# Performance work log

Hardware: AMD Instinct MI355X
Metric: run time of the kernel (lower is better)

Reference implementation:

```python
import jax, jax.numpy as jnp
import numpy as np

N_NODES = 20000
N_EDGES = 320000
X_DIM = 128
EDGE_DIM = 64
HIDDEN = 256
OUT_DIM = 256
LAYERS = 3
N_GRAPHS = 64


def setup_inputs() -> dict:
    key = jax.random.key(0)
    ks = jax.random.split(key, 20)
    x = jax.random.normal(ks[0], (N_NODES, X_DIM), dtype=jnp.float32)
    edge_index = jax.random.randint(ks[1], (2, N_EDGES), 0, N_NODES, dtype=jnp.int64)
    edge_attr = jax.random.normal(ks[2], (N_EDGES, EDGE_DIM), dtype=jnp.float32)
    batch_ids = jnp.sort(jax.random.randint(ks[3], (N_NODES,), 0, N_GRAPHS, dtype=jnp.int64))

    def lin(k, fan_in, fan_out):
        bound = 1.0 / np.sqrt(fan_in)
        kw, kb = jax.random.split(k)
        W = jax.random.uniform(kw, (fan_in, fan_out), minval=-bound, maxval=bound, dtype=jnp.float32)
        b = jax.random.uniform(kb, (fan_out,), minval=-bound, maxval=bound, dtype=jnp.float32)
        return W, b

    xproj_W, xproj_b = lin(ks[4], X_DIM, HIDDEN)
    edge_W, edge_b, mlp_W1, mlp_b1, mlp_W2, mlp_b2 = [], [], [], [], [], []
    for l in range(LAYERS):
        eW, eb = lin(ks[5 + l], EDGE_DIM, HIDDEN)
        w1, b1 = lin(ks[8 + l], HIDDEN, HIDDEN)
        w2, b2 = lin(ks[11 + l], HIDDEN, HIDDEN)
        edge_W.append(eW); edge_b.append(eb)
        mlp_W1.append(w1); mlp_b1.append(b1)
        mlp_W2.append(w2); mlp_b2.append(b2)
    out_W1, out_b1 = lin(ks[14], HIDDEN, HIDDEN)
    out_W2, out_b2 = lin(ks[15], HIDDEN, OUT_DIM)
    return {
        "x": x, "edge_index": edge_index, "edge_attr": edge_attr, "batch_ids": batch_ids,
        "xproj_W": xproj_W, "xproj_b": xproj_b,
        "edge_W": jnp.stack(edge_W), "edge_b": jnp.stack(edge_b),
        "mlp_W1": jnp.stack(mlp_W1), "mlp_b1": jnp.stack(mlp_b1),
        "mlp_W2": jnp.stack(mlp_W2), "mlp_b2": jnp.stack(mlp_b2),
        "out_W1": out_W1, "out_b1": out_b1, "out_W2": out_W2, "out_b2": out_b2,
    }


def reference(x, edge_index, edge_attr, batch_ids, xproj_W, xproj_b,
              edge_W, edge_b, mlp_W1, mlp_b1, mlp_W2, mlp_b2,
              out_W1, out_b1, out_W2, out_b2):
    src, dst = edge_index[0], edge_index[1]
    h = x @ xproj_W + xproj_b  # [N, H]
    for l in range(LAYERS):
        # GINE message: relu(x_j + Lin(edge_attr)), aggregated by sum at target
        msg = jax.nn.relu(h[src] + edge_attr @ edge_W[l] + edge_b[l])  # [E, H]
        agg = jax.ops.segment_sum(msg, dst, num_segments=N_NODES)      # [N, H]
        z = h + agg  # (1 + eps) * x_i with eps = 0
        z = jax.nn.relu(z @ mlp_W1[l] + mlp_b1[l]) @ mlp_W2[l] + mlp_b2[l]
        h = jax.nn.relu(z)  # outer F.relu in forward
    # global mean pool over graphs
    sums = jax.ops.segment_sum(h, batch_ids, num_segments=N_GRAPHS)    # [G, H]
    counts = jax.ops.segment_sum(jnp.ones((h.shape[0],), h.dtype), batch_ids, num_segments=N_GRAPHS)
    g = sums / jnp.maximum(counts, 1.0)[:, None]
    g = jax.nn.relu(g @ out_W1 + out_b1) @ out_W2 + out_b2
    # F.normalize(dim=-1): x / max(||x||_2, eps)
    norm = jnp.maximum(jnp.linalg.norm(g, axis=-1, keepdims=True), 1e-12)
    return g / norm
```

## Files before the change

kernel.cpp:

```cpp
#include <hip/hip_runtime.h>

#define N_NODES 20000
#define N_EDGES 320000
#define X_DIM 128
#define EDGE_DIM 64
#define HIDDEN 256
#define N_GRAPHS 64
#define LAYERS 3

#define NPB 8
#define EB 32
#define ET 4
#define PSPLIT 8
#define NBLK ((N_NODES + 255) / 256)

typedef __attribute__((ext_vector_type(8))) short short8;
typedef __attribute__((ext_vector_type(4))) float floatx4;

__device__ __forceinline__ unsigned short f2bf(float f) {
    union { float f; unsigned u; } v; v.f = f;
    return (unsigned short)((v.u + 0x7FFFu + ((v.u >> 16) & 1u)) >> 16);
}
__device__ __forceinline__ float bf2f(unsigned short u) {
    return __uint_as_float(((unsigned)u) << 16);
}


__global__ __launch_bounds__(256) void deg_kernel(const int* __restrict__ ei,
                                                  int* __restrict__ deg)
{
    int e = blockIdx.x * 256 + threadIdx.x;
    if (e < N_EDGES) atomicAdd(&deg[ei[N_EDGES + e]], 1);
}

__global__ __launch_bounds__(256) void pscan_kernel(const int* __restrict__ deg,
                                                    int* __restrict__ rp,
                                                    int* __restrict__ bsum)
{
    __shared__ int buf[256];
    const int t = threadIdx.x;
    const int i = blockIdx.x * 256 + t;
    int v = (i < N_NODES) ? deg[i] : 0;
    buf[t] = v;
    __syncthreads();
    for (int off = 1; off < 256; off <<= 1) {
        int a = (t >= off) ? buf[t - off] : 0;
        __syncthreads();
        buf[t] += a;
        __syncthreads();
    }
    if (i < N_NODES) rp[i] = buf[t] - v;
    if (t == 255) bsum[blockIdx.x] = buf[255];
}

__global__ __launch_bounds__(128) void bscan_kernel(const int* __restrict__ bsum,
                                                    int* __restrict__ boff)
{
    __shared__ int buf[128];
    const int t = threadIdx.x;
    int v = (t < NBLK) ? bsum[t] : 0;
    buf[t] = v;
    __syncthreads();
    for (int off = 1; off < 128; off <<= 1) {
        int a = (t >= off) ? buf[t - off] : 0;
        __syncthreads();
        buf[t] += a;
        __syncthreads();
    }
    if (t < NBLK) boff[t] = buf[t] - v;
}

__global__ __launch_bounds__(256) void addoff_kernel(int* __restrict__ rp,
                                                     const int* __restrict__ boff)
{
    const int i = blockIdx.x * 256 + threadIdx.x;
    if (i < N_NODES) rp[i] += boff[blockIdx.x];
    if (i == 0) rp[N_NODES] = N_EDGES;
}

__global__ __launch_bounds__(256) void scatter_kernel(const int* __restrict__ ei,
                                                      const int* __restrict__ rp,
                                                      int* __restrict__ cursor,
                                                      int* __restrict__ perm)
{
    const int e = blockIdx.x * 256 + threadIdx.x;
    if (e < N_EDGES) {
        const int d = ei[N_EDGES + e];
        const int pos = atomicAdd(&cursor[d], 1);
        perm[rp[d] + pos] = e;
    }
}

__global__ __launch_bounds__(256) void permute_kernel(
    const float* __restrict__ ea, const int* __restrict__ ei,
    const int* __restrict__ perm, unsigned short* __restrict__ eab,
    int* __restrict__ srcs, int* __restrict__ dsts)
{
    const int tid = blockIdx.x * 256 + threadIdx.x;
    const int e = tid >> 3, seg = tid & 7;
    const int p = perm[e];
    const float* sp = ea + (size_t)p * EDGE_DIM + seg * 8;
    const float4 v0 = *(const float4*)sp;
    const float4 v1 = *(const float4*)(sp + 4);
    short8 o;
    o[0] = (short)f2bf(v0.x); o[1] = (short)f2bf(v0.y);
    o[2] = (short)f2bf(v0.z); o[3] = (short)f2bf(v0.w);
    o[4] = (short)f2bf(v1.x); o[5] = (short)f2bf(v1.y);
    o[6] = (short)f2bf(v1.z); o[7] = (short)f2bf(v1.w);
    *(short8*)(eab + (size_t)e * EDGE_DIM + seg * 8) = o;
    if (seg == 0) { srcs[e] = ei[p]; dsts[e] = ei[N_EDGES + p]; }
}

__global__ __launch_bounds__(256) void swizzle_kernel(const float* __restrict__ W,
                                                      unsigned short* __restrict__ out,
                                                      int KK)
{
    const int i = blockIdx.x * 256 + threadIdx.x;
    if (i >= 8192 * KK) return;
    const int j = i & 7, lane = (i >> 3) & 63, rem = i >> 9;
    const int kk = rem % KK, rem2 = rem / KK, nt = rem2 & 3, wvv = rem2 >> 2;
    const int n = wvv * 64 + nt * 16 + (lane & 15);
    const int k = kk * 32 + (lane >> 4) * 8 + j;
    out[i] = f2bf(W[k * HIDDEN + n]);
}


__global__ __launch_bounds__(256) void node_proj_kernel(
    const float* __restrict__ x, const float* __restrict__ W,
    const float* __restrict__ b, float* __restrict__ h,
    unsigned short* __restrict__ hbf, float* __restrict__ z)
{
    const int t = threadIdx.x;
    const int row0 = blockIdx.x * NPB;
    __shared__ float xs[NPB][X_DIM];
    for (int idx = t; idx < NPB * X_DIM; idx += 256)
        xs[idx / X_DIM][idx % X_DIM] = x[(size_t)row0 * X_DIM + idx];
    __syncthreads();
    float acc[NPB];
    const float bt = b[t];
#pragma unroll
    for (int r = 0; r < NPB; r++) acc[r] = bt;
    for (int k = 0; k < X_DIM; k++) {
        const float wv = W[k * HIDDEN + t];
#pragma unroll
        for (int r = 0; r < NPB; r++) acc[r] += xs[r][k] * wv;
    }
#pragma unroll
    for (int r = 0; r < NPB; r++) {
        const size_t idx = (size_t)(row0 + r) * HIDDEN + t;
        h[idx] = acc[r];
        hbf[idx] = f2bf(acc[r]);
        z[idx] = 0.f;
    }
}

__global__ __launch_bounds__(256, 4) void edge_mfma_kernel(
    const unsigned short* __restrict__ eab, const int* __restrict__ srcs,
    const int* __restrict__ dsts, const unsigned short* __restrict__ Ws,
    const float* __restrict__ b, const unsigned short* __restrict__ hbf,
    float* __restrict__ z)
{
    const int t = threadIdx.x;
    const int lane = t & 63, wv = t >> 6, q = lane >> 4, m15 = lane & 15;
    __shared__ unsigned short msg[EB][264];
    __shared__ int s_src[2][EB], s_dst[2][EB];

    short8 bfr[4][2];
#pragma unroll
    for (int nt = 0; nt < 4; nt++)
#pragma unroll
        for (int kk = 0; kk < 2; kk++)
            bfr[nt][kk] = *(const short8*)(Ws + ((((wv * 4 + nt) * 2 + kk) * 64) + lane) * 8);
    const float bt = b[t];

    if (t < EB) {
        const int e0 = blockIdx.x * ET * EB;
        s_src[0][t] = srcs[e0 + t];
        s_dst[0][t] = dsts[e0 + t];
    }
    __syncthreads();

    float s = 0.f;
    int prev = s_dst[0][0];

    for (int tile = 0; tile < ET; tile++) {
        const int cur = tile & 1;
        const int e0 = (blockIdx.x * ET + tile) * EB;

        unsigned short hv[EB];
#pragma unroll
        for (int e = 0; e < EB; e++)
            hv[e] = hbf[(size_t)s_src[cur][e] * HIDDEN + t];

        if (tile + 1 < ET && t < EB) {
            s_src[1 - cur][t] = srcs[e0 + EB + t];
            s_dst[1 - cur][t] = dsts[e0 + EB + t];
        }

        floatx4 acc[2][4];
#pragma unroll
        for (int mt = 0; mt < 2; mt++)
#pragma unroll
            for (int nt = 0; nt < 4; nt++)
                acc[mt][nt] = (floatx4){0.f, 0.f, 0.f, 0.f};
#pragma unroll
        for (int kk = 0; kk < 2; kk++) {
            const short8 a0 = *(const short8*)(eab + (size_t)(e0 + m15) * EDGE_DIM + kk * 32 + q * 8);
            const short8 a1 = *(const short8*)(eab + (size_t)(e0 + 16 + m15) * EDGE_DIM + kk * 32 + q * 8);
#pragma unroll
            for (int nt = 0; nt < 4; nt++) {
                acc[0][nt] = __builtin_amdgcn_mfma_f32_16x16x32_bf16(a0, bfr[nt][kk], acc[0][nt], 0, 0, 0);
                acc[1][nt] = __builtin_amdgcn_mfma_f32_16x16x32_bf16(a1, bfr[nt][kk], acc[1][nt], 0, 0, 0);
            }
        }
#pragma unroll
        for (int mt = 0; mt < 2; mt++)
#pragma unroll
            for (int nt = 0; nt < 4; nt++)
#pragma unroll
                for (int r = 0; r < 4; r++)
                    msg[mt * 16 + q * 4 + r][wv * 64 + nt * 16 + m15] = f2bf(acc[mt][nt][r]);
        __syncthreads();

#pragma unroll
        for (int e = 0; e < EB; e++) {
            const int d = s_dst[cur][e];
            if (d != prev) {
                atomicAdd(&z[(size_t)prev * HIDDEN + t], s);
                s = 0.f; prev = d;
            }
            const float m = bf2f(msg[e][t]) + bt + bf2f(hv[e]);
            s += m > 0.f ? m : 0.f;
        }
        __syncthreads();
    }
    atomicAdd(&z[(size_t)prev * HIDDEN + t], s);
}

__global__ __launch_bounds__(256) void mlp_mfma_kernel(
    const unsigned short* __restrict__ W1s, const float* __restrict__ b1,
    const unsigned short* __restrict__ W2s, const float* __restrict__ b2,
    float* __restrict__ h, float* __restrict__ z, unsigned short* __restrict__ hbf)
{
    const int t = threadIdx.x;
    const int lane = t & 63, wv = t >> 6, q = lane >> 4, m15 = lane & 15;
    const int row0 = blockIdx.x * 32;
    __shared__ __align__(16) unsigned short zs[32][264];

#pragma unroll
    for (int r = 0; r < 32; r++) {
        const size_t idx = (size_t)(row0 + r) * HIDDEN + t;
        zs[r][t] = f2bf(h[idx] + z[idx]);
        z[idx] = 0.f;
    }
    __syncthreads();

    float b1v[4], b2v[4];
#pragma unroll
    for (int nt = 0; nt < 4; nt++) {
        const int c = wv * 64 + nt * 16 + m15;
        b1v[nt] = b1[c]; b2v[nt] = b2[c];
    }

    floatx4 acc[2][4];
#pragma unroll
    for (int mt = 0; mt < 2; mt++)
#pragma unroll
        for (int nt = 0; nt < 4; nt++)
            acc[mt][nt] = (floatx4){0.f, 0.f, 0.f, 0.f};

#pragma unroll
    for (int kk = 0; kk < 8; kk++) {
        short8 bfr[4];
#pragma unroll
        for (int nt = 0; nt < 4; nt++)
            bfr[nt] = *(const short8*)(W1s + ((((wv * 4 + nt) * 8 + kk) * 64) + lane) * 8);
        const short8 a0 = *(const short8*)&zs[m15][kk * 32 + q * 8];
        const short8 a1 = *(const short8*)&zs[16 + m15][kk * 32 + q * 8];
#pragma unroll
        for (int nt = 0; nt < 4; nt++) {
            acc[0][nt] = __builtin_amdgcn_mfma_f32_16x16x32_bf16(a0, bfr[nt], acc[0][nt], 0, 0, 0);
            acc[1][nt] = __builtin_amdgcn_mfma_f32_16x16x32_bf16(a1, bfr[nt], acc[1][nt], 0, 0, 0);
        }
    }
    __syncthreads();
#pragma unroll
    for (int mt = 0; mt < 2; mt++)
#pragma unroll
        for (int nt = 0; nt < 4; nt++)
#pragma unroll
            for (int r = 0; r < 4; r++) {
                const int row = mt * 16 + q * 4 + r, c = wv * 64 + nt * 16 + m15;
                const float v = acc[mt][nt][r] + b1v[nt];
                zs[row][c] = f2bf(v > 0.f ? v : 0.f);
            }
    __syncthreads();

#pragma unroll
    for (int mt = 0; mt < 2; mt++)
#pragma unroll
        for (int nt = 0; nt < 4; nt++)
            acc[mt][nt] = (floatx4){0.f, 0.f, 0.f, 0.f};

#pragma unroll
    for (int kk = 0; kk < 8; kk++) {
        short8 bfr[4];
#pragma unroll
        for (int nt = 0; nt < 4; nt++)
            bfr[nt] = *(const short8*)(W2s + ((((wv * 4 + nt) * 8 + kk) * 64) + lane) * 8);
        const short8 a0 = *(const short8*)&zs[m15][kk * 32 + q * 8];
        const short8 a1 = *(const short8*)&zs[16 + m15][kk * 32 + q * 8];
#pragma unroll
        for (int nt = 0; nt < 4; nt++) {
            acc[0][nt] = __builtin_amdgcn_mfma_f32_16x16x32_bf16(a0, bfr[nt], acc[0][nt], 0, 0, 0);
            acc[1][nt] = __builtin_amdgcn_mfma_f32_16x16x32_bf16(a1, bfr[nt], acc[1][nt], 0, 0, 0);
        }
    }
#pragma unroll
    for (int mt = 0; mt < 2; mt++)
#pragma unroll
        for (int nt = 0; nt < 4; nt++)
#pragma unroll
            for (int r = 0; r < 4; r++) {
                const int row = mt * 16 + q * 4 + r, c = wv * 64 + nt * 16 + m15;
                float v = acc[mt][nt][r] + b2v[nt];
                v = v > 0.f ? v : 0.f;
                const size_t idx = (size_t)(row0 + row) * HIDDEN + c;
                h[idx] = v;
                hbf[idx] = f2bf(v);
            }
}

__global__ __launch_bounds__(256) void pool_kernel(
    const float* __restrict__ h, const int* __restrict__ bid,
    float* __restrict__ gsum)
{
    const int g = blockIdx.x / PSPLIT;
    const int part = blockIdx.x % PSPLIT;
    const int t = threadIdx.x;
    int lo = 0, hi = N_NODES;
    while (lo < hi) { int mid = (lo + hi) >> 1; if (bid[mid] < g) lo = mid + 1; else hi = mid; }
    const int start = lo;
    hi = N_NODES;
    while (lo < hi) { int mid = (lo + hi) >> 1; if (bid[mid] < g + 1) lo = mid + 1; else hi = mid; }
    const int end = lo;
    const int len = end - start;
    const int chunk = (len + PSPLIT - 1) / PSPLIT;
    const int s0 = start + part * chunk;
    const int s1 = min(s0 + chunk, end);
    if (s0 >= s1) return;
    float s = 0.f;
    for (int i = s0; i < s1; i++) s += h[(size_t)i * HIDDEN + t];
    atomicAdd(&gsum[g * HIDDEN + t], s);
}

__global__ __launch_bounds__(256) void head_kernel(
    const float* __restrict__ gsum, const int* __restrict__ bid,
    const float* __restrict__ W1, const float* __restrict__ b1,
    const float* __restrict__ W2, const float* __restrict__ b2,
    float* __restrict__ out)
{
    const int g = blockIdx.x;
    const int t = threadIdx.x;
    __shared__ float gs[HIDDEN];
    __shared__ float t1[HIDDEN];
    __shared__ float red[256];
    int lo = 0, hi = N_NODES;
    while (lo < hi) { int mid = (lo + hi) >> 1; if (bid[mid] < g) lo = mid + 1; else hi = mid; }
    const int start = lo;
    hi = N_NODES;
    while (lo < hi) { int mid = (lo + hi) >> 1; if (bid[mid] < g + 1) lo = mid + 1; else hi = mid; }
    float cnt = (float)(lo - start);
    cnt = cnt > 1.f ? cnt : 1.f;
    gs[t] = gsum[g * HIDDEN + t] / cnt;
    __syncthreads();
    float acc = b1[t];
    for (int k = 0; k < HIDDEN; k++) acc += gs[k] * W1[k * HIDDEN + t];
    t1[t] = acc > 0.f ? acc : 0.f;
    __syncthreads();
    float acc2 = b2[t];
    for (int k = 0; k < HIDDEN; k++) acc2 += t1[k] * W2[k * HIDDEN + t];
    red[t] = acc2 * acc2;
    __syncthreads();
    for (int s = 128; s > 0; s >>= 1) {
        if (t < s) red[t] += red[t + s];
        __syncthreads();
    }
    float norm = sqrtf(red[0]);
    norm = norm > 1e-12f ? norm : 1e-12f;
    out[g * HIDDEN + t] = acc2 / norm;
}

extern "C" void kernel_launch(void* const* d_in, const int* in_sizes, int n_in,
                              void* d_out, int out_size, void* d_ws, size_t ws_size,
                              hipStream_t stream)
{
    const float* x   = (const float*)d_in[0];
    const int*   ei  = (const int*)d_in[1];
    const float* ea  = (const float*)d_in[2];
    const int*   bid = (const int*)d_in[3];
    const float* xW  = (const float*)d_in[4];
    const float* xb  = (const float*)d_in[5];
    const float* eW  = (const float*)d_in[6];
    const float* eb  = (const float*)d_in[7];
    const float* W1  = (const float*)d_in[8];
    const float* b1  = (const float*)d_in[9];
    const float* W2  = (const float*)d_in[10];
    const float* b2  = (const float*)d_in[11];
    const float* oW1 = (const float*)d_in[12];
    const float* ob1 = (const float*)d_in[13];
    const float* oW2 = (const float*)d_in[14];
    const float* ob2 = (const float*)d_in[15];
    float* out = (float*)d_out;

    char* p = (char*)d_ws;
    auto alloc = [&](size_t bytes) { char* r = p; p += (bytes + 255) & ~(size_t)255; return r; };
    float* h     = (float*)alloc((size_t)N_NODES * HIDDEN * 4);
    float* z     = (float*)alloc((size_t)N_NODES * HIDDEN * 4);
    float* gpool = (float*)alloc((size_t)N_GRAPHS * HIDDEN * 4);
    int* deg     = (int*)alloc(N_NODES * 4);
    int* rowptr  = (int*)alloc((N_NODES + 1) * 4);
    int* cursor  = (int*)alloc(N_NODES * 4);
    int* bsum    = (int*)alloc(NBLK * 4);
    int* boff    = (int*)alloc(NBLK * 4);
    int* perm    = (int*)alloc((size_t)N_EDGES * 4);
    int* srcs    = (int*)alloc((size_t)N_EDGES * 4);
    int* dsts    = (int*)alloc((size_t)N_EDGES * 4);
    unsigned short* hbf = (unsigned short*)alloc((size_t)N_NODES * HIDDEN * 2);
    unsigned short* eab = (unsigned short*)alloc((size_t)N_EDGES * EDGE_DIM * 2);
    unsigned short* eWs = (unsigned short*)alloc((size_t)LAYERS * EDGE_DIM * HIDDEN * 2);
    unsigned short* W1s = (unsigned short*)alloc((size_t)LAYERS * HIDDEN * HIDDEN * 2);
    unsigned short* W2s = (unsigned short*)alloc((size_t)LAYERS * HIDDEN * HIDDEN * 2);

    hipMemsetAsync(deg, 0, N_NODES * sizeof(int), stream);
    hipMemsetAsync(cursor, 0, N_NODES * sizeof(int), stream);
    hipMemsetAsync(gpool, 0, N_GRAPHS * HIDDEN * sizeof(float), stream);
    deg_kernel<<<(N_EDGES + 255) / 256, 256, 0, stream>>>(ei, deg);
    pscan_kernel<<<NBLK, 256, 0, stream>>>(deg, rowptr, bsum);
    bscan_kernel<<<1, 128, 0, stream>>>(bsum, boff);
    addoff_kernel<<<NBLK, 256, 0, stream>>>(rowptr, boff);
    scatter_kernel<<<(N_EDGES + 255) / 256, 256, 0, stream>>>(ei, rowptr, cursor, perm);
    permute_kernel<<<(N_EDGES * 8) / 256, 256, 0, stream>>>(ea, ei, perm, eab, srcs, dsts);
    for (int l = 0; l < LAYERS; l++) {
        swizzle_kernel<<<64, 256, 0, stream>>>(eW + (size_t)l * EDGE_DIM * HIDDEN,
                                               eWs + (size_t)l * EDGE_DIM * HIDDEN, 2);
        swizzle_kernel<<<256, 256, 0, stream>>>(W1 + (size_t)l * HIDDEN * HIDDEN,
                                                W1s + (size_t)l * HIDDEN * HIDDEN, 8);
        swizzle_kernel<<<256, 256, 0, stream>>>(W2 + (size_t)l * HIDDEN * HIDDEN,
                                                W2s + (size_t)l * HIDDEN * HIDDEN, 8);
    }

    node_proj_kernel<<<N_NODES / NPB, 256, 0, stream>>>(x, xW, xb, h, hbf, z);
    for (int l = 0; l < LAYERS; l++) {
        edge_mfma_kernel<<<N_EDGES / (EB * ET), 256, 0, stream>>>(
            eab, srcs, dsts, eWs + (size_t)l * EDGE_DIM * HIDDEN,
            eb + l * HIDDEN, hbf, z);
        mlp_mfma_kernel<<<N_NODES / 32, 256, 0, stream>>>(
            W1s + (size_t)l * HIDDEN * HIDDEN, b1 + l * HIDDEN,
            W2s + (size_t)l * HIDDEN * HIDDEN, b2 + l * HIDDEN, h, z, hbf);
    }
    pool_kernel<<<N_GRAPHS * PSPLIT, 256, 0, stream>>>(h, bid, gpool);
    head_kernel<<<N_GRAPHS, 256, 0, stream>>>(gpool, bid, oW1, ob1, oW2, ob2, out);
}
```

Measured before the change: 603.7 us.

## Partition edge aggregation by destination node blocks, drop atomics and z buffer

The edge kernel now assigns each block a contiguous range of 16 destination nodes and walks their CSR edge range, summing messages into a shared-memory accumulator seeded with h. It then writes h+agg as bf16 for the MLP kernel. This removes global float atomics, the z zero-fill, and the fp32 z read in the MLP. Bias is folded into the MFMA accumulator init, and the per-layer swizzle launches are merged into single launches. The cost is load imbalance from variable degree per block and some wasted work on partial tiles. There is also a possible race: sidx is written per wavefront while other waves read msg without a block barrier.

```diff
diff --git a/kernel.cpp b/kernel.cpp
--- a/kernel.cpp
+++ b/kernel.cpp
@@ -10,7 +10,7 @@
 
 #define NPB 8
 #define EB 32
-#define ET 4
+#define NB 16
 #define PSPLIT 8
 #define NBLK ((N_NODES + 255) / 256)
 
@@ -113,22 +113,24 @@
 
 __global__ __launch_bounds__(256) void swizzle_kernel(const float* __restrict__ W,
                                                       unsigned short* __restrict__ out,
-                                                      int KK)
-{
-    const int i = blockIdx.x * 256 + threadIdx.x;
-    if (i >= 8192 * KK) return;
+                                                      int KK, int total)
+{
+    const int gi = blockIdx.x * 256 + threadIdx.x;
+    if (gi >= total) return;
+    const int per = 8192 * KK;
+    const int l = gi / per, i = gi % per;
     const int j = i & 7, lane = (i >> 3) & 63, rem = i >> 9;
     const int kk = rem % KK, rem2 = rem / KK, nt = rem2 & 3, wvv = rem2 >> 2;
     const int n = wvv * 64 + nt * 16 + (lane & 15);
     const int k = kk * 32 + (lane >> 4) * 8 + j;
-    out[i] = f2bf(W[k * HIDDEN + n]);
+    out[(size_t)l * per + i] = f2bf(W[(size_t)l * per + k * HIDDEN + n]);
 }
 
 
 __global__ __launch_bounds__(256) void node_proj_kernel(
     const float* __restrict__ x, const float* __restrict__ W,
     const float* __restrict__ b, float* __restrict__ h,
-    unsigned short* __restrict__ hbf, float* __restrict__ z)
+    unsigned short* __restrict__ hbf)
 {
     const int t = threadIdx.x;
     const int row0 = blockIdx.x * NPB;
@@ -150,20 +152,27 @@
         const size_t idx = (size_t)(row0 + r) * HIDDEN + t;
         h[idx] = acc[r];
         hbf[idx] = f2bf(acc[r]);
-        z[idx] = 0.f;
     }
 }
 
 __global__ __launch_bounds__(256, 4) void edge_mfma_kernel(
     const unsigned short* __restrict__ eab, const int* __restrict__ srcs,
-    const int* __restrict__ dsts, const unsigned short* __restrict__ Ws,
-    const float* __restrict__ b, const unsigned short* __restrict__ hbf,
-    float* __restrict__ z)
+    const int* __restrict__ dsts, const int* __restrict__ rowptr,
+    const unsigned short* __restrict__ Ws, const float* __restrict__ b,
+    const unsigned short* __restrict__ hbf, const float* __restrict__ h,
+    unsigned short* __restrict__ Abf)
 {
     const int t = threadIdx.x;
     const int lane = t & 63, wv = t >> 6, q = lane >> 4, m15 = lane & 15;
-    __shared__ unsigned short msg[EB][264];
-    __shared__ int s_src[2][EB], s_dst[2][EB];
+    const int row0 = blockIdx.x * NB;
+
+    __shared__ float agg[NB][HIDDEN];
+    __shared__ unsigned short msg[EB][260];
+    __shared__ int sidx[4][2][2][32];
+
+#pragma unroll
+    for (int r = 0; r < NB; r++)
+        agg[r][t] = h[(size_t)(row0 + r) * HIDDEN + t];
 
     short8 bfr[4][2];
 #pragma unroll
@@ -171,87 +180,104 @@
 #pragma unroll
         for (int kk = 0; kk < 2; kk++)
             bfr[nt][kk] = *(const short8*)(Ws + ((((wv * 4 + nt) * 2 + kk) * 64) + lane) * 8);
-    const float bt = b[t];
-
-    if (t < EB) {
-        const int e0 = blockIdx.x * ET * EB;
-        s_src[0][t] = srcs[e0 + t];
-        s_dst[0][t] = dsts[e0 + t];
-    }
-    __syncthreads();
-
+    float bv[4];
+#pragma unroll
+    for (int nt = 0; nt < 4; nt++) bv[nt] = b[wv * 64 + nt * 16 + m15];
+
+    const int e_start = rowptr[row0];
+    const int e_end   = rowptr[row0 + NB];
+    const int cnt = e_end - e_start;
+    const int ntiles = (cnt + EB - 1) >> 5;
+
+    if (lane < 32) {
+        int eg = e_start + lane; eg = eg < N_EDGES ? eg : N_EDGES - 1;
+        sidx[wv][0][0][lane] = srcs[eg];
+        sidx[wv][0][1][lane] = dsts[eg];
+    }
+    int prev = 0;
     float s = 0.f;
-    int prev = s_dst[0][0];
-
-    for (int tile = 0; tile < ET; tile++) {
+    if (cnt > 0) prev = sidx[wv][0][1][0];
+
+    for (int tile = 0; tile < ntiles; tile++) {
         const int cur = tile & 1;
-        const int e0 = (blockIdx.x * ET + tile) * EB;
+        const int ebase = e_start + tile * EB;
+        const int nin = min(EB, e_end - ebase);
+
+        short8 a0[2], a1[2];
+#pragma unroll
+        for (int kk = 0; kk < 2; kk++) {
+            a0[kk] = *(const short8*)(eab + (size_t)(ebase + m15) * EDGE_DIM + kk * 32 + q * 8);
+            a1[kk] = *(const short8*)(eab + (size_t)(ebase + 16 + m15) * EDGE_DIM + kk * 32 + q * 8);
+        }
 
         unsigned short hv[EB];
 #pragma unroll
         for (int e = 0; e < EB; e++)
-            hv[e] = hbf[(size_t)s_src[cur][e] * HIDDEN + t];
-
-        if (tile + 1 < ET && t < EB) {
-            s_src[1 - cur][t] = srcs[e0 + EB + t];
-            s_dst[1 - cur][t] = dsts[e0 + EB + t];
-        }
-
-        floatx4 acc[2][4];
-#pragma unroll
-        for (int mt = 0; mt < 2; mt++)
+            hv[e] = hbf[(size_t)sidx[wv][cur][0][e] * HIDDEN + t];
+
+        if (tile + 1 < ntiles && lane < 32) {
+            int eg = ebase + EB + lane; eg = eg < N_EDGES ? eg : N_EDGES - 1;
+            sidx[wv][1 - cur][0][lane] = srcs[eg];
+            sidx[wv][1 - cur][1][lane] = dsts[eg];
+        }
+
+#pragma unroll
+        for (int mt = 0; mt < 2; mt++) {
+            floatx4 acc[4];
 #pragma unroll
             for (int nt = 0; nt < 4; nt++)
-                acc[mt][nt] = (floatx4){0.f, 0.f, 0.f, 0.f};
-#pragma unroll
-        for (int kk = 0; kk < 2; kk++) {
-            const short8 a0 = *(const short8*)(eab + (size_t)(e0 + m15) * EDGE_DIM + kk * 32 + q * 8);
-            const short8 a1 = *(const short8*)(eab + (size_t)(e0 + 16 + m15) * EDGE_DIM + kk * 32 + q * 8);
-#pragma unroll
-            for (int nt = 0; nt < 4; nt++) {
-                acc[0][nt] = __builtin_amdgcn_mfma_f32_16x16x32_bf16(a0, bfr[nt][kk], acc[0][nt], 0, 0, 0);
-                acc[1][nt] = __builtin_amdgcn_mfma_f32_16x16x32_bf16(a1, bfr[nt][kk], acc[1][nt], 0, 0, 0);
+                acc[nt] = (floatx4){bv[nt], bv[nt], bv[nt], bv[nt]};
+#pragma unroll
+            for (int kk = 0; kk < 2; kk++) {
+                const short8 a = mt ? a1[kk] : a0[kk];
+#pragma unroll
+                for (int nt = 0; nt < 4; nt++)
+                    acc[nt] = __builtin_amdgcn_mfma_f32_16x16x32_bf16(a, bfr[nt][kk], acc[nt], 0, 0, 0);
             }
-        }
-#pragma unroll
-        for (int mt = 0; mt < 2; mt++)
 #pragma unroll
             for (int nt = 0; nt < 4; nt++)
 #pragma unroll
                 for (int r = 0; r < 4; r++)
-                    msg[mt * 16 + q * 4 + r][wv * 64 + nt * 16 + m15] = f2bf(acc[mt][nt][r]);
-        __syncthreads();
+                    msg[mt * 16 + q * 4 + r][wv * 64 + nt * 16 + m15] = f2bf(acc[nt][r]);
+        }
 
 #pragma unroll
         for (int e = 0; e < EB; e++) {
-            const int d = s_dst[cur][e];
-            if (d != prev) {
-                atomicAdd(&z[(size_t)prev * HIDDEN + t], s);
-                s = 0.f; prev = d;
+            if (e < nin) {
+                const int d = sidx[wv][cur][1][e];
+                if (d != prev) {
+                    agg[prev - row0][t] += s;
+                    s = 0.f; prev = d;
+                }
+                const float m = bf2f(msg[e][t]) + bf2f(hv[e]);
+                s += m > 0.f ? m : 0.f;
             }
-            const float m = bf2f(msg[e][t]) + bt + bf2f(hv[e]);
-            s += m > 0.f ? m : 0.f;
-        }
-        __syncthreads();
-    }
-    atomicAdd(&z[(size_t)prev * HIDDEN + t], s);
+        }
+    }
+    if (cnt > 0) agg[prev - row0][t] += s;
+
+#pragma unroll
+    for (int r = 0; r < NB; r++)
+        Abf[(size_t)(row0 + r) * HIDDEN + t] = f2bf(agg[r][t]);
 }
 
 __global__ __launch_bounds__(256) void mlp_mfma_kernel(
     const unsigned short* __restrict__ W1s, const float* __restrict__ b1,
     const unsigned short* __restrict__ W2s, const float* __restrict__ b2,
-    float* __restrict__ h, float* __restrict__ z, unsigned short* __restrict__ hbf)
+    const unsigned short* __restrict__ Abf,
+    float* __restrict__ h, unsigned short* __restrict__ hbf)
 {
     const int t = threadIdx.x;
     const int lane = t & 63, wv = t >> 6, q = lane >> 4, m15 = lane & 15;
     const int row0 = blockIdx.x * 32;
     __shared__ __align__(16) unsigned short zs[32][264];
 
-#pragma unroll
-    for (int r = 0; r < 32; r++) {
-        const size_t idx = (size_t)(row0 + r) * HIDDEN + t;
-        zs[r][t] = f2bf(h[idx] + z[idx]);
-        z[idx] = 0.f;
+    const size_t base = (size_t)row0 * HIDDEN;
+#pragma unroll
+    for (int i = 0; i < 4; i++) {
+        const int idx = i * 256 + t;
+        const int row = idx >> 5, col = idx & 31;
+        *(short8*)&zs[row][col * 8] = *(const short8*)(Abf + base + (size_t)idx * 8);
     }
     __syncthreads();
 
@@ -416,7 +442,6 @@
     char* p = (char*)d_ws;
     auto alloc = [&](size_t bytes) { char* r = p; p += (bytes + 255) & ~(size_t)255; return r; };
     float* h     = (float*)alloc((size_t)N_NODES * HIDDEN * 4);
-    float* z     = (float*)alloc((size_t)N_NODES * HIDDEN * 4);
     float* gpool = (float*)alloc((size_t)N_GRAPHS * HIDDEN * 4);
     int* deg     = (int*)alloc(N_NODES * 4);
     int* rowptr  = (int*)alloc((N_NODES + 1) * 4);
@@ -427,7 +452,8 @@
     int* srcs    = (int*)alloc((size_t)N_EDGES * 4);
     int* dsts    = (int*)alloc((size_t)N_EDGES * 4);
     unsigned short* hbf = (unsigned short*)alloc((size_t)N_NODES * HIDDEN * 2);
-    unsigned short* eab = (unsigned short*)alloc((size_t)N_EDGES * EDGE_DIM * 2);
+    unsigned short* Abf = (unsigned short*)alloc((size_t)N_NODES * HIDDEN * 2);
+    unsigned short* eab = (unsigned short*)alloc((size_t)(N_EDGES + EB) * EDGE_DIM * 2);
     unsigned short* eWs = (unsigned short*)alloc((size_t)LAYERS * EDGE_DIM * HIDDEN * 2);
     unsigned short* W1s = (unsigned short*)alloc((size_t)LAYERS * HIDDEN * HIDDEN * 2);
     unsigned short* W2s = (unsigned short*)alloc((size_t)LAYERS * HIDDEN * HIDDEN * 2);
@@ -441,23 +467,18 @@
     addoff_kernel<<<NBLK, 256, 0, stream>>>(rowptr, boff);
     scatter_kernel<<<(N_EDGES + 255) / 256, 256, 0, stream>>>(ei, rowptr, cursor, perm);
     permute_kernel<<<(N_EDGES * 8) / 256, 256, 0, stream>>>(ea, ei, perm, eab, srcs, dsts);
+    swizzle_kernel<<<(LAYERS * 8192 * 2 + 255) / 256, 256, 0, stream>>>(eW, eWs, 2, LAYERS * 8192 * 2);
+    swizzle_kernel<<<(LAYERS * 8192 * 8 + 255) / 256, 256, 0, stream>>>(W1, W1s, 8, LAYERS * 8192 * 8);
+    swizzle_kernel<<<(LAYERS * 8192 * 8 + 255) / 256, 256, 0, stream>>>(W2, W2s, 8, LAYERS * 8192 * 8);
+
+    node_proj_kernel<<<N_NODES / NPB, 256, 0, stream>>>(x, xW, xb, h, hbf);
     for (int l = 0; l < LAYERS; l++) {
-        swizzle_kernel<<<64, 256, 0, stream>>>(eW + (size_t)l * EDGE_DIM * HIDDEN,
-                                               eWs + (size_t)l * EDGE_DIM * HIDDEN, 2);
-        swizzle_kernel<<<256, 256, 0, stream>>>(W1 + (size_t)l * HIDDEN * HIDDEN,
-                                                W1s + (size_t)l * HIDDEN * HIDDEN, 8);
-        swizzle_kernel<<<256, 256, 0, stream>>>(W2 + (size_t)l * HIDDEN * HIDDEN,
-                                                W2s + (size_t)l * HIDDEN * HIDDEN, 8);
-    }
-
-    node_proj_kernel<<<N_NODES / NPB, 256, 0, stream>>>(x, xW, xb, h, hbf, z);
-    for (int l = 0; l < LAYERS; l++) {
-        edge_mfma_kernel<<<N_EDGES / (EB * ET), 256, 0, stream>>>(
-            eab, srcs, dsts, eWs + (size_t)l * EDGE_DIM * HIDDEN,
-            eb + l * HIDDEN, hbf, z);
+        edge_mfma_kernel<<<N_NODES / NB, 256, 0, stream>>>(
+            eab, srcs, dsts, rowptr, eWs + (size_t)l * EDGE_DIM * HIDDEN,
+            eb + l * HIDDEN, hbf, h, Abf);
         mlp_mfma_kernel<<<N_NODES / 32, 256, 0, stream>>>(
             W1s + (size_t)l * HIDDEN * HIDDEN, b1 + l * HIDDEN,
-            W2s + (size_t)l * HIDDEN * HIDDEN, b2 + l * HIDDEN, h, z, hbf);
+            W2s + (size_t)l * HIDDEN * HIDDEN, b2 + l * HIDDEN, Abf, h, hbf);
     }
     pool_kernel<<<N_GRAPHS * PSPLIT, 256, 0, stream>>>(h, bid, gpool);
     head_kernel<<<N_GRAPHS, 256, 0, stream>>>(gpool, bid, oW1, ob1, oW2, ob2, out);
```

New measurement: 595.9 us. No clear change (-1.3%).
